# Kernel optimization log

Measured on AMD Instinct MI355X. Metric: run time of the kernel, lower is better.

## Reference

```python
import jax, jax.numpy as jnp
import numpy as np

B, H, E, V, T, EOS = 128, 512, 256, 32000, 32, 0

def setup_inputs() -> dict:
    key = jax.random.key(0)
    ks = jax.random.split(key, 10)
    s_emb = 1.0 / np.sqrt(V)
    s_rnn = 1.0 / np.sqrt(H)
    return {
        "z": jax.random.normal(ks[0], (B, H), jnp.float32),
        "W_emb": jax.random.uniform(ks[1], (E, V), jnp.float32, -s_emb, s_emb),
        "b_emb": jax.random.uniform(ks[2], (E,), jnp.float32, -s_emb, s_emb),
        "W_ih": jax.random.uniform(ks[3], (H, E), jnp.float32, -s_rnn, s_rnn),
        "b_ih": jax.random.uniform(ks[4], (H,), jnp.float32, -s_rnn, s_rnn),
        "W_hh": jax.random.uniform(ks[5], (H, H), jnp.float32, -s_rnn, s_rnn),
        "b_hh": jax.random.uniform(ks[6], (H,), jnp.float32, -s_rnn, s_rnn),
        "W_lin": jax.random.uniform(ks[7], (V, H), jnp.float32, -s_rnn, s_rnn),
        "b_lin": jax.random.uniform(ks[8], (V,), jnp.float32, -s_rnn, s_rnn),
        "train": 0,
    }

def _emit(hidden, W_lin, b_lin):
    # [B,H] @ [H,V] -> log_p [B,V]; greedy (argmax) decode path (train=False)
    log_p = jax.nn.log_softmax(hidden @ W_lin.T + b_lin, axis=-1)
    sample = jnp.argmax(log_p, axis=-1)                       # [B] int
    symb = jax.nn.one_hot(sample, V, dtype=log_p.dtype)       # [B,V]
    lp_tok = jnp.take_along_axis(log_p, sample[:, None], axis=1)[:, 0]
    return symb, lp_tok

def reference(z, W_emb, b_emb, W_ih, b_ih, W_hh, b_hh, W_lin, b_lin, train):
    # step 0: hidden = z, no RNN update
    symb, lp_tok = _emit(z, W_lin, b_lin)
    log_p_sent = lp_tok
    mask = 1.0 - symb[:, EOS]

    def step(carry, _):
        hidden, symb, log_p_sent, mask = carry
        emb = symb @ W_emb.T + b_emb                          # one-hot "embedding" linear
        hidden = jnp.tanh(emb @ W_ih.T + b_ih + hidden @ W_hh.T + b_hh)  # Elman RNN cell
        symb, lp_tok = _emit(hidden, W_lin, b_lin)
        log_p_sent = log_p_sent + mask * lp_tok
        mask = mask * (1.0 - symb[:, EOS])
        return (hidden, symb, log_p_sent, mask), symb

    (_, _, log_p_sent, _), rest = jax.lax.scan(step, (z, symb, log_p_sent, mask), None, length=T - 1)
    sentences = jnp.concatenate([symb[None], rest], axis=0)   # [T,B,V]
    return sentences, log_p_sent
```

## Files before the change

kernel.cpp:

```cpp
#include <hip/hip_runtime.h>
#include <math.h>

constexpr int NB = 128;
constexpr int NH = 512;
constexpr int NE = 256;
constexpr int NV = 32000;
constexpr int NT = 32;
constexpr int NVBW = 1000;

typedef _Float16 half8 __attribute__((ext_vector_type(8)));
typedef float    f32x4 __attribute__((ext_vector_type(4)));

__global__ void f32_to_f16_kernel(const float* __restrict__ src,
                                  _Float16* __restrict__ dst, int n8)
{
    int i = blockIdx.x * 256 + threadIdx.x;
    if (i >= n8) return;
    float4 a = ((const float4*)src)[i * 2];
    float4 b = ((const float4*)src)[i * 2 + 1];
    half8 h = { (_Float16)a.x, (_Float16)a.y, (_Float16)a.z, (_Float16)a.w,
                (_Float16)b.x, (_Float16)b.y, (_Float16)b.z, (_Float16)b.w };
    ((half8*)dst)[i] = h;
}

__global__ __launch_bounds__(512, 1)
void logits_kernel(const _Float16* __restrict__ Ah,
                   const _Float16* __restrict__ Wh,
                   const float* __restrict__ blin,
                   float* __restrict__ pm1, int* __restrict__ pi1,
                   float* __restrict__ pm2, int* __restrict__ pi2,
                   float* __restrict__ ps)
{
    __shared__ _Float16 sm[2][2][128][64];

    const int tid  = threadIdx.x;
    const int w    = tid >> 6;
    const int lane = tid & 63;
    const int wm   = w >> 2;
    const int wn   = w & 3;
    const int vb   = blockIdx.x;
    const int v0   = vb * 128;

    const _Float16* gp[4];
    unsigned ldsoff[4];
#pragma unroll
    for (int c = 0; c < 4; c++) {
        int slot = w * 256 + c * 64 + lane;
        int mat  = slot >> 10;
        int r    = (slot >> 3) & 127;
        int sp   = slot & 7;
        int s    = sp ^ (r & 7);
        const _Float16* base = mat ? (Wh + (size_t)(v0 + r) * NH)
                                   : (Ah + (size_t)r * NH);
        gp[c] = base + s * 8;
        ldsoff[c] = (unsigned)(w * 256 + c * 64) * 16;
    }

#define STAGE(db, k0)                                                          \
    do {                                                                       \
        _Pragma("unroll")                                                      \
        for (int c = 0; c < 4; c++) {                                          \
            __builtin_amdgcn_global_load_lds(                                  \
                (const __attribute__((address_space(1))) unsigned*)(gp[c] + (k0)), \
                (__attribute__((address_space(3))) unsigned*)((char*)&sm[db][0][0][0] + ldsoff[c]), \
                16, 0, 0);                                                     \
        }                                                                      \
    } while (0)

    f32x4 acc[4][2];
#pragma unroll
    for (int mi = 0; mi < 4; mi++)
#pragma unroll
        for (int ni = 0; ni < 2; ni++) acc[mi][ni] = {0.f, 0.f, 0.f, 0.f};

    STAGE(0, 0);
    asm volatile("s_waitcnt vmcnt(0)" ::: "memory");
    __builtin_amdgcn_sched_barrier(0);
    __builtin_amdgcn_s_barrier();

    int db = 0;
    for (int t = 0; t < 8; t++) {
        if (t < 7) STAGE(db ^ 1, (t + 1) * 64);
#pragma unroll
        for (int kk = 0; kk < 2; kk++) {
            const int sbase = kk * 4 + (lane >> 4);
            half8 af[4], bf[2];
#pragma unroll
            for (int mi = 0; mi < 4; mi++) {
                int r = wm * 64 + mi * 16 + (lane & 15);
                af[mi] = *(const half8*)&sm[db][0][r][(sbase ^ (r & 7)) * 8];
            }
#pragma unroll
            for (int ni = 0; ni < 2; ni++) {
                int rb = wn * 32 + ni * 16 + (lane & 15);
                bf[ni] = *(const half8*)&sm[db][1][rb][(sbase ^ (rb & 7)) * 8];
            }
#pragma unroll
            for (int mi = 0; mi < 4; mi++)
#pragma unroll
                for (int ni = 0; ni < 2; ni++)
                    acc[mi][ni] = __builtin_amdgcn_mfma_f32_16x16x32_f16(
                        af[mi], bf[ni], acc[mi][ni], 0, 0, 0);
        }
        asm volatile("s_waitcnt vmcnt(0)" ::: "memory");
        __builtin_amdgcn_sched_barrier(0);
        __builtin_amdgcn_s_barrier();
        db ^= 1;
    }
#undef STAGE

    const int colbase = v0 + wn * 32 + (lane & 15);
    const float bias0 = blin[colbase];
    const float bias1 = blin[colbase + 16];
    const int cidx = vb * 4 + wn;

#pragma unroll
    for (int mi = 0; mi < 4; mi++) {
#pragma unroll
        for (int reg = 0; reg < 4; reg++) {
            const int b = wm * 64 + mi * 16 + (lane >> 4) * 4 + reg;
            const float va = acc[mi][0][reg] + bias0;
            const float vc = acc[mi][1][reg] + bias1;
            float a1, a2; int j1, j2;
            if (va >= vc) { a1 = va; j1 = colbase;      a2 = vc; j2 = colbase + 16; }
            else          { a1 = vc; j1 = colbase + 16; a2 = va; j2 = colbase; }
#pragma unroll
            for (int off = 1; off < 16; off <<= 1) {
                float o1 = __shfl_xor(a1, off), o2 = __shfl_xor(a2, off);
                int   k1 = __shfl_xor(j1, off), k2 = __shfl_xor(j2, off);
                float n1, n2; int m1, m2;
                bool ob = (o1 > a1) || (o1 == a1 && k1 < j1);
                if (ob) {
                    n1 = o1; m1 = k1;
                    bool t2 = (a1 > o2) || (a1 == o2 && j1 < k2);
                    if (t2) { n2 = a1; m2 = j1; } else { n2 = o2; m2 = k2; }
                } else {
                    n1 = a1; m1 = j1;
                    bool t2 = (o1 > a2) || (o1 == a2 && k1 < j2);
                    if (t2) { n2 = o1; m2 = k1; } else { n2 = a2; m2 = j2; }
                }
                a1 = n1; j1 = m1; a2 = n2; j2 = m2;
            }
            float s = __expf(va - a1) + __expf(vc - a1);
#pragma unroll
            for (int off = 1; off < 16; off <<= 1) s += __shfl_xor(s, off);
            if ((lane & 15) == 0) {
                pm1[b * NVBW + cidx] = a1;  pi1[b * NVBW + cidx] = j1;
                pm2[b * NVBW + cidx] = a2;  pi2[b * NVBW + cidx] = j2;
                ps [b * NVBW + cidx] = s;
            }
        }
    }
}

__global__ __launch_bounds__(256, 2)
void emit_rnn_kernel(int t,
                     const float* __restrict__ hid_in,
                     const float* __restrict__ Wlin, const float* __restrict__ blin,
                     const float* __restrict__ pm1, const int* __restrict__ pi1,
                     const float* __restrict__ pm2, const int* __restrict__ pi2,
                     const float* __restrict__ ps,
                     const float* __restrict__ Wemb, const float* __restrict__ bemb,
                     const float* __restrict__ Wih, const float* __restrict__ bih,
                     const float* __restrict__ Whh, const float* __restrict__ bhh,
                     float* __restrict__ hid_out, _Float16* __restrict__ hidh_out,
                     float* __restrict__ lps, float* __restrict__ maskp,
                     float* __restrict__ out)
{
    constexpr float DELTA = 0.01f;
    constexpr int   MAXC  = 32;

    const int b = blockIdx.x, tid = threadIdx.x;
    const int w = tid >> 6, lane = tid & 63;

    __shared__ float red[4];
    __shared__ int   cand[MAXC];
    __shared__ float cval[MAXC];
    __shared__ int   ncand;
    __shared__ int   besti;
    __shared__ float es[NE];
    __shared__ float hs[NH];

    hs[tid]       = hid_in[(size_t)b * NH + tid];
    hs[tid + 256] = hid_in[(size_t)b * NH + tid + 256];
    if (tid == 0) ncand = 0;

    float m = -1e30f;
    for (int c = tid; c < NVBW; c += 256) m = fmaxf(m, pm1[b * NVBW + c]);
#pragma unroll
    for (int off = 1; off < 64; off <<= 1) m = fmaxf(m, __shfl_xor(m, off));
    if (lane == 0) red[w] = m;
    __syncthreads();
    const float gm = fmaxf(fmaxf(red[0], red[1]), fmaxf(red[2], red[3]));
    __syncthreads();

    float s = 0.f;
    for (int c = tid; c < NVBW; c += 256) {
        float p1 = pm1[b * NVBW + c];
        s += ps[b * NVBW + c] * __expf(p1 - gm);
        if (p1 >= gm - DELTA) {
            int pos = atomicAdd(&ncand, 1);
            if (pos < MAXC) cand[pos] = pi1[b * NVBW + c];
        }
        float p2 = pm2[b * NVBW + c];
        if (p2 >= gm - DELTA) {
            int pos = atomicAdd(&ncand, 1);
            if (pos < MAXC) cand[pos] = pi2[b * NVBW + c];
        }
    }
#pragma unroll
    for (int off = 1; off < 64; off <<= 1) s += __shfl_xor(s, off);
    if (lane == 0) red[w] = s;
    __syncthreads();
    const float tot = red[0] + red[1] + red[2] + red[3];
    const int nc = min(ncand, MAXC);

    for (int ci = w; ci < nc; ci += 4) {
        int tok = cand[ci];
        float4 h0 = ((const float4*)hs)[lane * 2];
        float4 h1 = ((const float4*)hs)[lane * 2 + 1];
        const float4* wv = (const float4*)(Wlin + (size_t)tok * NH);
        float4 w0 = wv[lane * 2], w1 = wv[lane * 2 + 1];
        float d = h0.x * w0.x + h0.y * w0.y + h0.z * w0.z + h0.w * w0.w
                + h1.x * w1.x + h1.y * w1.y + h1.z * w1.z + h1.w * w1.w;
#pragma unroll
        for (int off = 1; off < 64; off <<= 1) d += __shfl_xor(d, off);
        if (lane == 0) cval[ci] = d + blin[tok];
    }
    __syncthreads();

    if (tid == 0) {
        float bv = cval[0]; int bi = cand[0];
        for (int ci = 1; ci < nc; ci++)
            if (cval[ci] > bv || (cval[ci] == bv && cand[ci] < bi)) { bv = cval[ci]; bi = cand[ci]; }
        float lp = (bv - gm) - logf(tot);
        float lpv, mk;
        if (t == 0) { lpv = lp; mk = (bi == 0) ? 0.f : 1.f; }
        else {
            lpv = lps[b]; mk = maskp[b];
            lpv += mk * lp;
            mk *= (bi == 0) ? 0.f : 1.f;
        }
        lps[b] = lpv; maskp[b] = mk;
        out[(size_t)t * NB * NV + (size_t)b * NV + bi] = 1.0f;
        if (t == NT - 1) out[(size_t)NT * NB * NV + b] = lpv;
        besti = bi;
    }
    __syncthreads();
    const int gi = besti;

    if (t == NT - 1) return;

    es[tid] = Wemb[(size_t)tid * NV + gi] + bemb[tid];
    __syncthreads();

#pragma unroll
    for (int hh = 0; hh < 2; hh++) {
        int h = tid + hh * 256;
        float acc = bih[h] + bhh[h];
        const float4* wi = (const float4*)(Wih + (size_t)h * NE);
#pragma unroll 4
        for (int e4 = 0; e4 < NE / 4; e4++) {
            float4 ww = wi[e4];
            acc += ww.x * es[e4 * 4] + ww.y * es[e4 * 4 + 1]
                 + ww.z * es[e4 * 4 + 2] + ww.w * es[e4 * 4 + 3];
        }
        const float4* wh = (const float4*)(Whh + (size_t)h * NH);
#pragma unroll 4
        for (int k4 = 0; k4 < NH / 4; k4++) {
            float4 ww = wh[k4];
            acc += ww.x * hs[k4 * 4] + ww.y * hs[k4 * 4 + 1]
                 + ww.z * hs[k4 * 4 + 2] + ww.w * hs[k4 * 4 + 3];
        }
        float v = tanhf(acc);
        hid_out[(size_t)b * NH + h]  = v;
        hidh_out[(size_t)b * NH + h] = (_Float16)v;
    }
}

extern "C" void kernel_launch(void* const* d_in, const int* in_sizes, int n_in,
                              void* d_out, int out_size, void* d_ws, size_t ws_size,
                              hipStream_t stream) {
    const float* z    = (const float*)d_in[0];
    const float* Wemb = (const float*)d_in[1];
    const float* bemb = (const float*)d_in[2];
    const float* Wih  = (const float*)d_in[3];
    const float* bih  = (const float*)d_in[4];
    const float* Whh  = (const float*)d_in[5];
    const float* bhh  = (const float*)d_in[6];
    const float* Wlin = (const float*)d_in[7];
    const float* blin = (const float*)d_in[8];
    float* out = (float*)d_out;

    char* ws = (char*)d_ws;
    _Float16* Wh    = (_Float16*)(ws);
    _Float16* hidh  = (_Float16*)(ws + 32768000);
    _Float16* zh    = (_Float16*)(ws + 32899072);
    float*    hid   = (float*)   (ws + 33030144);
    float*    pm1   = (float*)   (ws + 33292288);
    int*      pi1   = (int*)     (ws + 33804288);
    float*    pm2   = (float*)   (ws + 34316288);
    int*      pi2   = (int*)     (ws + 34828288);
    float*    ps    = (float*)   (ws + 35340288);
    float*    lps   = (float*)   (ws + 35852288);
    float*    maskp = (float*)   (ws + 35852800);

    hipMemsetAsync(d_out, 0, (size_t)NT * NB * NV * sizeof(float), stream);
    f32_to_f16_kernel<<<NV * NH / 8 / 256, 256, 0, stream>>>(Wlin, Wh, NV * NH / 8);
    f32_to_f16_kernel<<<NB * NH / 8 / 256, 256, 0, stream>>>(z, zh, NB * NH / 8);

    for (int t = 0; t < NT; t++) {
        const float*    hin = (t == 0) ? z  : hid;
        const _Float16* ah  = (t == 0) ? zh : hidh;
        logits_kernel<<<250, 512, 0, stream>>>(ah, Wh, blin, pm1, pi1, pm2, pi2, ps);
        emit_rnn_kernel<<<NB, 256, 0, stream>>>(t, hin, Wlin, blin,
                                                pm1, pi1, pm2, pi2, ps,
                                                Wemb, bemb, Wih, bih, Whh, bhh,
                                                hid, hidh, lps, maskp, out);
    }
}
```

Before: 2.992 ms.

## Fuse all decode steps into one persistent cooperative kernel with grid syncs

Replaces the memset, two conversion kernels and 64 per-step launches with a single cooperative kernel of 256 blocks. The blocks zero the output, convert weights to fp16, and then loop over the timesteps, with grid-wide syncs separating the logits GEMM phase from the emit/RNN phase. This removes kernel launch gaps and the per-step launch overhead. In exchange it adds grid-sync latency and narrows the emit phase to 512-thread blocks doing one hidden unit per thread. It also requires that all 256 blocks be co-resident.

```diff
diff --git a/kernel.cpp b/kernel.cpp
--- a/kernel.cpp
+++ b/kernel.cpp
@@ -1,5 +1,8 @@
 #include <hip/hip_runtime.h>
+#include <hip/hip_cooperative_groups.h>
 #include <math.h>
+
+namespace cg = cooperative_groups;
 
 constexpr int NB = 128;
 constexpr int NH = 512;
@@ -11,50 +14,82 @@
 typedef _Float16 half8 __attribute__((ext_vector_type(8)));
 typedef float    f32x4 __attribute__((ext_vector_type(4)));
 
-__global__ void f32_to_f16_kernel(const float* __restrict__ src,
-                                  _Float16* __restrict__ dst, int n8)
+__global__ __launch_bounds__(512, 2)
+void speaker_kernel(const float* __restrict__ z,    const float* __restrict__ Wemb,
+                    const float* __restrict__ bemb, const float* __restrict__ Wih,
+                    const float* __restrict__ bih,  const float* __restrict__ Whh,
+                    const float* __restrict__ bhh,  const float* __restrict__ Wlin,
+                    const float* __restrict__ blin, float* __restrict__ out,
+                    _Float16* __restrict__ Wh, _Float16* __restrict__ hidh,
+                    _Float16* __restrict__ zh, float* __restrict__ hid,
+                    float* __restrict__ pm1, int* __restrict__ pi1,
+                    float* __restrict__ pm2, int* __restrict__ pi2,
+                    float* __restrict__ ps,  float* __restrict__ lps,
+                    float* __restrict__ maskp)
 {
-    int i = blockIdx.x * 256 + threadIdx.x;
-    if (i >= n8) return;
-    float4 a = ((const float4*)src)[i * 2];
-    float4 b = ((const float4*)src)[i * 2 + 1];
-    half8 h = { (_Float16)a.x, (_Float16)a.y, (_Float16)a.z, (_Float16)a.w,
-                (_Float16)b.x, (_Float16)b.y, (_Float16)b.z, (_Float16)b.w };
-    ((half8*)dst)[i] = h;
-}
-
-__global__ __launch_bounds__(512, 1)
-void logits_kernel(const _Float16* __restrict__ Ah,
-                   const _Float16* __restrict__ Wh,
-                   const float* __restrict__ blin,
-                   float* __restrict__ pm1, int* __restrict__ pi1,
-                   float* __restrict__ pm2, int* __restrict__ pi2,
-                   float* __restrict__ ps)
-{
+    cg::grid_group grid = cg::this_grid();
+
     __shared__ _Float16 sm[2][2][128][64];
-
+    __shared__ float red8[8];
+    __shared__ int   cand[32];
+    __shared__ float cval[32];
+    __shared__ int   ncand;
+    __shared__ int   besti;
+    __shared__ float es[NE];
+    __shared__ float hs[NH];
+
+    const int blk  = blockIdx.x;
     const int tid  = threadIdx.x;
+    const int gtid = blk * 512 + tid;
+    constexpr int GT = 256 * 512;
+
+    {
+        const float4 z4 = {0.f, 0.f, 0.f, 0.f};
+        float4* o4 = (float4*)out;
+        for (int i = gtid; i < (NT * NB * NV + NB) / 4; i += GT) o4[i] = z4;
+        for (int i = gtid; i < NV * NH / 8; i += GT) {
+            float4 a = ((const float4*)Wlin)[i * 2];
+            float4 b = ((const float4*)Wlin)[i * 2 + 1];
+            half8 h = { (_Float16)a.x, (_Float16)a.y, (_Float16)a.z, (_Float16)a.w,
+                        (_Float16)b.x, (_Float16)b.y, (_Float16)b.z, (_Float16)b.w };
+            ((half8*)Wh)[i] = h;
+        }
+        for (int i = gtid; i < NB * NH / 8; i += GT) {
+            float4 a = ((const float4*)z)[i * 2];
+            float4 b = ((const float4*)z)[i * 2 + 1];
+            half8 h = { (_Float16)a.x, (_Float16)a.y, (_Float16)a.z, (_Float16)a.w,
+                        (_Float16)b.x, (_Float16)b.y, (_Float16)b.z, (_Float16)b.w };
+            ((half8*)zh)[i] = h;
+        }
+    }
+    __threadfence();
+    grid.sync();
+
     const int w    = tid >> 6;
     const int lane = tid & 63;
-    const int wm   = w >> 2;
-    const int wn   = w & 3;
-    const int vb   = blockIdx.x;
-    const int v0   = vb * 128;
-
-    const _Float16* gp[4];
-    unsigned ldsoff[4];
-#pragma unroll
-    for (int c = 0; c < 4; c++) {
-        int slot = w * 256 + c * 64 + lane;
-        int mat  = slot >> 10;
-        int r    = (slot >> 3) & 127;
-        int sp   = slot & 7;
-        int s    = sp ^ (r & 7);
-        const _Float16* base = mat ? (Wh + (size_t)(v0 + r) * NH)
-                                   : (Ah + (size_t)r * NH);
-        gp[c] = base + s * 8;
-        ldsoff[c] = (unsigned)(w * 256 + c * 64) * 16;
-    }
+
+    for (int t = 0; t < NT; t++) {
+        if (blk < 250) {
+            const _Float16* Ah = (t == 0) ? zh : hidh;
+            const int wm = w >> 2;
+            const int wn = w & 3;
+            const int vb = blk;
+            const int v0 = vb * 128;
+
+            const _Float16* gp[4];
+            unsigned ldsoff[4];
+#pragma unroll
+            for (int c = 0; c < 4; c++) {
+                int slot = w * 256 + c * 64 + lane;
+                int mat  = slot >> 10;
+                int r    = (slot >> 3) & 127;
+                int sp   = slot & 7;
+                int s    = sp ^ (r & 7);
+                const _Float16* base = mat ? (Wh + (size_t)(v0 + r) * NH)
+                                           : (Ah + (size_t)r * NH);
+                gp[c] = base + s * 8;
+                ldsoff[c] = (unsigned)(w * 256 + c * 64) * 16;
+            }
 
 #define STAGE(db, k0)                                                          \
     do {                                                                       \
@@ -67,214 +102,197 @@
         }                                                                      \
     } while (0)
 
-    f32x4 acc[4][2];
-#pragma unroll
-    for (int mi = 0; mi < 4; mi++)
-#pragma unroll
-        for (int ni = 0; ni < 2; ni++) acc[mi][ni] = {0.f, 0.f, 0.f, 0.f};
-
-    STAGE(0, 0);
-    asm volatile("s_waitcnt vmcnt(0)" ::: "memory");
-    __builtin_amdgcn_sched_barrier(0);
-    __builtin_amdgcn_s_barrier();
-
-    int db = 0;
-    for (int t = 0; t < 8; t++) {
-        if (t < 7) STAGE(db ^ 1, (t + 1) * 64);
-#pragma unroll
-        for (int kk = 0; kk < 2; kk++) {
-            const int sbase = kk * 4 + (lane >> 4);
-            half8 af[4], bf[2];
+            f32x4 acc[4][2];
+#pragma unroll
+            for (int mi = 0; mi < 4; mi++)
+#pragma unroll
+                for (int ni = 0; ni < 2; ni++) acc[mi][ni] = {0.f, 0.f, 0.f, 0.f};
+
+            STAGE(0, 0);
+            asm volatile("s_waitcnt vmcnt(0)" ::: "memory");
+            __builtin_amdgcn_sched_barrier(0);
+            __builtin_amdgcn_s_barrier();
+
+            int db = 0;
+            for (int kt = 0; kt < 8; kt++) {
+                if (kt < 7) STAGE(db ^ 1, (kt + 1) * 64);
+#pragma unroll
+                for (int kk = 0; kk < 2; kk++) {
+                    const int sbase = kk * 4 + (lane >> 4);
+                    half8 af[4], bf[2];
+#pragma unroll
+                    for (int mi = 0; mi < 4; mi++) {
+                        int r = wm * 64 + mi * 16 + (lane & 15);
+                        af[mi] = *(const half8*)&sm[db][0][r][(sbase ^ (r & 7)) * 8];
+                    }
+#pragma unroll
+                    for (int ni = 0; ni < 2; ni++) {
+                        int rb = wn * 32 + ni * 16 + (lane & 15);
+                        bf[ni] = *(const half8*)&sm[db][1][rb][(sbase ^ (rb & 7)) * 8];
+                    }
+#pragma unroll
+                    for (int mi = 0; mi < 4; mi++)
+#pragma unroll
+                        for (int ni = 0; ni < 2; ni++)
+                            acc[mi][ni] = __builtin_amdgcn_mfma_f32_16x16x32_f16(
+                                af[mi], bf[ni], acc[mi][ni], 0, 0, 0);
+                }
+                asm volatile("s_waitcnt vmcnt(0)" ::: "memory");
+                __builtin_amdgcn_sched_barrier(0);
+                __builtin_amdgcn_s_barrier();
+                db ^= 1;
+            }
+#undef STAGE
+
+            const int colbase = v0 + wn * 32 + (lane & 15);
+            const float bias0 = blin[colbase];
+            const float bias1 = blin[colbase + 16];
+            const int cidx = vb * 4 + wn;
+
 #pragma unroll
             for (int mi = 0; mi < 4; mi++) {
-                int r = wm * 64 + mi * 16 + (lane & 15);
-                af[mi] = *(const half8*)&sm[db][0][r][(sbase ^ (r & 7)) * 8];
-            }
-#pragma unroll
-            for (int ni = 0; ni < 2; ni++) {
-                int rb = wn * 32 + ni * 16 + (lane & 15);
-                bf[ni] = *(const half8*)&sm[db][1][rb][(sbase ^ (rb & 7)) * 8];
-            }
-#pragma unroll
-            for (int mi = 0; mi < 4; mi++)
-#pragma unroll
-                for (int ni = 0; ni < 2; ni++)
-                    acc[mi][ni] = __builtin_amdgcn_mfma_f32_16x16x32_f16(
-                        af[mi], bf[ni], acc[mi][ni], 0, 0, 0);
+#pragma unroll
+                for (int reg = 0; reg < 4; reg++) {
+                    const int b = wm * 64 + mi * 16 + (lane >> 4) * 4 + reg;
+                    const float va = acc[mi][0][reg] + bias0;
+                    const float vc = acc[mi][1][reg] + bias1;
+                    float a1, a2; int j1, j2;
+                    if (va >= vc) { a1 = va; j1 = colbase;      a2 = vc; j2 = colbase + 16; }
+                    else          { a1 = vc; j1 = colbase + 16; a2 = va; j2 = colbase; }
+#pragma unroll
+                    for (int off = 1; off < 16; off <<= 1) {
+                        float o1 = __shfl_xor(a1, off), o2 = __shfl_xor(a2, off);
+                        int   k1 = __shfl_xor(j1, off), k2 = __shfl_xor(j2, off);
+                        float n1, n2; int m1, m2;
+                        bool ob = (o1 > a1) || (o1 == a1 && k1 < j1);
+                        if (ob) {
+                            n1 = o1; m1 = k1;
+                            bool t2 = (a1 > o2) || (a1 == o2 && j1 < k2);
+                            if (t2) { n2 = a1; m2 = j1; } else { n2 = o2; m2 = k2; }
+                        } else {
+                            n1 = a1; m1 = j1;
+                            bool t2 = (o1 > a2) || (o1 == a2 && k1 < j2);
+                            if (t2) { n2 = o1; m2 = k1; } else { n2 = a2; m2 = j2; }
+                        }
+                        a1 = n1; j1 = m1; a2 = n2; j2 = m2;
+                    }
+                    float s = __expf(va - a1) + __expf(vc - a1);
+#pragma unroll
+                    for (int off = 1; off < 16; off <<= 1) s += __shfl_xor(s, off);
+                    if ((lane & 15) == 0) {
+                        pm1[b * NVBW + cidx] = a1;  pi1[b * NVBW + cidx] = j1;
+                        pm2[b * NVBW + cidx] = a2;  pi2[b * NVBW + cidx] = j2;
+                        ps [b * NVBW + cidx] = s;
+                    }
+                }
+            }
         }
-        asm volatile("s_waitcnt vmcnt(0)" ::: "memory");
-        __builtin_amdgcn_sched_barrier(0);
-        __builtin_amdgcn_s_barrier();
-        db ^= 1;
-    }
-#undef STAGE
-
-    const int colbase = v0 + wn * 32 + (lane & 15);
-    const float bias0 = blin[colbase];
-    const float bias1 = blin[colbase + 16];
-    const int cidx = vb * 4 + wn;
-
-#pragma unroll
-    for (int mi = 0; mi < 4; mi++) {
-#pragma unroll
-        for (int reg = 0; reg < 4; reg++) {
-            const int b = wm * 64 + mi * 16 + (lane >> 4) * 4 + reg;
-            const float va = acc[mi][0][reg] + bias0;
-            const float vc = acc[mi][1][reg] + bias1;
-            float a1, a2; int j1, j2;
-            if (va >= vc) { a1 = va; j1 = colbase;      a2 = vc; j2 = colbase + 16; }
-            else          { a1 = vc; j1 = colbase + 16; a2 = va; j2 = colbase; }
-#pragma unroll
-            for (int off = 1; off < 16; off <<= 1) {
-                float o1 = __shfl_xor(a1, off), o2 = __shfl_xor(a2, off);
-                int   k1 = __shfl_xor(j1, off), k2 = __shfl_xor(j2, off);
-                float n1, n2; int m1, m2;
-                bool ob = (o1 > a1) || (o1 == a1 && k1 < j1);
-                if (ob) {
-                    n1 = o1; m1 = k1;
-                    bool t2 = (a1 > o2) || (a1 == o2 && j1 < k2);
-                    if (t2) { n2 = a1; m2 = j1; } else { n2 = o2; m2 = k2; }
-                } else {
-                    n1 = a1; m1 = j1;
-                    bool t2 = (o1 > a2) || (o1 == a2 && k1 < j2);
-                    if (t2) { n2 = o1; m2 = k1; } else { n2 = a2; m2 = j2; }
-                }
-                a1 = n1; j1 = m1; a2 = n2; j2 = m2;
-            }
-            float s = __expf(va - a1) + __expf(vc - a1);
-#pragma unroll
-            for (int off = 1; off < 16; off <<= 1) s += __shfl_xor(s, off);
-            if ((lane & 15) == 0) {
-                pm1[b * NVBW + cidx] = a1;  pi1[b * NVBW + cidx] = j1;
-                pm2[b * NVBW + cidx] = a2;  pi2[b * NVBW + cidx] = j2;
-                ps [b * NVBW + cidx] = s;
+        __threadfence();
+        grid.sync();
+
+        if (blk < NB) {
+            constexpr float DELTA = 0.01f;
+            constexpr int   MAXC  = 32;
+            const int b = blk;
+            const float* hid_in = (t == 0) ? z : hid;
+
+            hs[tid] = hid_in[(size_t)b * NH + tid];
+            if (tid == 0) ncand = 0;
+            __syncthreads();
+
+            float m_ = -1e30f;
+            for (int c = tid; c < NVBW; c += 512) m_ = fmaxf(m_, pm1[b * NVBW + c]);
+#pragma unroll
+            for (int off = 1; off < 64; off <<= 1) m_ = fmaxf(m_, __shfl_xor(m_, off));
+            if (lane == 0) red8[w] = m_;
+            __syncthreads();
+            const float gmax = fmaxf(fmaxf(fmaxf(red8[0], red8[1]), fmaxf(red8[2], red8[3])),
+                                     fmaxf(fmaxf(red8[4], red8[5]), fmaxf(red8[6], red8[7])));
+            __syncthreads();
+
+            float s = 0.f;
+            for (int c = tid; c < NVBW; c += 512) {
+                float p1 = pm1[b * NVBW + c];
+                s += ps[b * NVBW + c] * __expf(p1 - gmax);
+                if (p1 >= gmax - DELTA) {
+                    int pos = atomicAdd(&ncand, 1);
+                    if (pos < MAXC) cand[pos] = pi1[b * NVBW + c];
+                }
+                float p2 = pm2[b * NVBW + c];
+                if (p2 >= gmax - DELTA) {
+                    int pos = atomicAdd(&ncand, 1);
+                    if (pos < MAXC) cand[pos] = pi2[b * NVBW + c];
+                }
+            }
+#pragma unroll
+            for (int off = 1; off < 64; off <<= 1) s += __shfl_xor(s, off);
+            if (lane == 0) red8[w] = s;
+            __syncthreads();
+            const float tot = ((red8[0] + red8[1]) + (red8[2] + red8[3]))
+                            + ((red8[4] + red8[5]) + (red8[6] + red8[7]));
+            const int nc = min(ncand, MAXC);
+
+            for (int ci = w; ci < nc; ci += 8) {
+                int tok = cand[ci];
+                float4 h0 = ((const float4*)hs)[lane * 2];
+                float4 h1 = ((const float4*)hs)[lane * 2 + 1];
+                const float4* wv = (const float4*)(Wlin + (size_t)tok * NH);
+                float4 w0 = wv[lane * 2], w1 = wv[lane * 2 + 1];
+                float d = h0.x * w0.x + h0.y * w0.y + h0.z * w0.z + h0.w * w0.w
+                        + h1.x * w1.x + h1.y * w1.y + h1.z * w1.z + h1.w * w1.w;
+#pragma unroll
+                for (int off = 1; off < 64; off <<= 1) d += __shfl_xor(d, off);
+                if (lane == 0) cval[ci] = d + blin[tok];
+            }
+            __syncthreads();
+
+            if (tid == 0) {
+                float bv = cval[0]; int bi = cand[0];
+                for (int ci = 1; ci < nc; ci++)
+                    if (cval[ci] > bv || (cval[ci] == bv && cand[ci] < bi)) { bv = cval[ci]; bi = cand[ci]; }
+                float lp = (bv - gmax) - logf(tot);
+                float lpv, mk;
+                if (t == 0) { lpv = lp; mk = (bi == 0) ? 0.f : 1.f; }
+                else {
+                    lpv = lps[b]; mk = maskp[b];
+                    lpv += mk * lp;
+                    mk *= (bi == 0) ? 0.f : 1.f;
+                }
+                lps[b] = lpv; maskp[b] = mk;
+                out[(size_t)t * NB * NV + (size_t)b * NV + bi] = 1.0f;
+                if (t == NT - 1) out[(size_t)NT * NB * NV + b] = lpv;
+                besti = bi;
+            }
+            __syncthreads();
+            const int gi = besti;
+
+            if (t < NT - 1) {
+                if (tid < NE) es[tid] = Wemb[(size_t)tid * NV + gi] + bemb[tid];
+                __syncthreads();
+
+                const int h = tid;
+                float acc = bih[h] + bhh[h];
+                const float4* wi = (const float4*)(Wih + (size_t)h * NE);
+#pragma unroll 4
+                for (int e4 = 0; e4 < NE / 4; e4++) {
+                    float4 ww = wi[e4];
+                    acc += ww.x * es[e4 * 4] + ww.y * es[e4 * 4 + 1]
+                         + ww.z * es[e4 * 4 + 2] + ww.w * es[e4 * 4 + 3];
+                }
+                const float4* wh = (const float4*)(Whh + (size_t)h * NH);
+#pragma unroll 4
+                for (int k4 = 0; k4 < NH / 4; k4++) {
+                    float4 ww = wh[k4];
+                    acc += ww.x * hs[k4 * 4] + ww.y * hs[k4 * 4 + 1]
+                         + ww.z * hs[k4 * 4 + 2] + ww.w * hs[k4 * 4 + 3];
+                }
+                float v = tanhf(acc);
+                hid[(size_t)b * NH + h]  = v;
+                hidh[(size_t)b * NH + h] = (_Float16)v;
             }
         }
-    }
-}
-
-__global__ __launch_bounds__(256, 2)
-void emit_rnn_kernel(int t,
-                     const float* __restrict__ hid_in,
-                     const float* __restrict__ Wlin, const float* __restrict__ blin,
-                     const float* __restrict__ pm1, const int* __restrict__ pi1,
-                     const float* __restrict__ pm2, const int* __restrict__ pi2,
-                     const float* __restrict__ ps,
-                     const float* __restrict__ Wemb, const float* __restrict__ bemb,
-                     const float* __restrict__ Wih, const float* __restrict__ bih,
-                     const float* __restrict__ Whh, const float* __restrict__ bhh,
-                     float* __restrict__ hid_out, _Float16* __restrict__ hidh_out,
-                     float* __restrict__ lps, float* __restrict__ maskp,
-                     float* __restrict__ out)
-{
-    constexpr float DELTA = 0.01f;
-    constexpr int   MAXC  = 32;
-
-    const int b = blockIdx.x, tid = threadIdx.x;
-    const int w = tid >> 6, lane = tid & 63;
-
-    __shared__ float red[4];
-    __shared__ int   cand[MAXC];
-    __shared__ float cval[MAXC];
-    __shared__ int   ncand;
-    __shared__ int   besti;
-    __shared__ float es[NE];
-    __shared__ float hs[NH];
-
-    hs[tid]       = hid_in[(size_t)b * NH + tid];
-    hs[tid + 256] = hid_in[(size_t)b * NH + tid + 256];
-    if (tid == 0) ncand = 0;
-
-    float m = -1e30f;
-    for (int c = tid; c < NVBW; c += 256) m = fmaxf(m, pm1[b * NVBW + c]);
-#pragma unroll
-    for (int off = 1; off < 64; off <<= 1) m = fmaxf(m, __shfl_xor(m, off));
-    if (lane == 0) red[w] = m;
-    __syncthreads();
-    const float gm = fmaxf(fmaxf(red[0], red[1]), fmaxf(red[2], red[3]));
-    __syncthreads();
-
-    float s = 0.f;
-    for (int c = tid; c < NVBW; c += 256) {
-        float p1 = pm1[b * NVBW + c];
-        s += ps[b * NVBW + c] * __expf(p1 - gm);
-        if (p1 >= gm - DELTA) {
-            int pos = atomicAdd(&ncand, 1);
-            if (pos < MAXC) cand[pos] = pi1[b * NVBW + c];
-        }
-        float p2 = pm2[b * NVBW + c];
-        if (p2 >= gm - DELTA) {
-            int pos = atomicAdd(&ncand, 1);
-            if (pos < MAXC) cand[pos] = pi2[b * NVBW + c];
-        }
-    }
-#pragma unroll
-    for (int off = 1; off < 64; off <<= 1) s += __shfl_xor(s, off);
-    if (lane == 0) red[w] = s;
-    __syncthreads();
-    const float tot = red[0] + red[1] + red[2] + red[3];
-    const int nc = min(ncand, MAXC);
-
-    for (int ci = w; ci < nc; ci += 4) {
-        int tok = cand[ci];
-        float4 h0 = ((const float4*)hs)[lane * 2];
-        float4 h1 = ((const float4*)hs)[lane * 2 + 1];
-        const float4* wv = (const float4*)(Wlin + (size_t)tok * NH);
-        float4 w0 = wv[lane * 2], w1 = wv[lane * 2 + 1];
-        float d = h0.x * w0.x + h0.y * w0.y + h0.z * w0.z + h0.w * w0.w
-                + h1.x * w1.x + h1.y * w1.y + h1.z * w1.z + h1.w * w1.w;
-#pragma unroll
-        for (int off = 1; off < 64; off <<= 1) d += __shfl_xor(d, off);
-        if (lane == 0) cval[ci] = d + blin[tok];
-    }
-    __syncthreads();
-
-    if (tid == 0) {
-        float bv = cval[0]; int bi = cand[0];
-        for (int ci = 1; ci < nc; ci++)
-            if (cval[ci] > bv || (cval[ci] == bv && cand[ci] < bi)) { bv = cval[ci]; bi = cand[ci]; }
-        float lp = (bv - gm) - logf(tot);
-        float lpv, mk;
-        if (t == 0) { lpv = lp; mk = (bi == 0) ? 0.f : 1.f; }
-        else {
-            lpv = lps[b]; mk = maskp[b];
-            lpv += mk * lp;
-            mk *= (bi == 0) ? 0.f : 1.f;
-        }
-        lps[b] = lpv; maskp[b] = mk;
-        out[(size_t)t * NB * NV + (size_t)b * NV + bi] = 1.0f;
-        if (t == NT - 1) out[(size_t)NT * NB * NV + b] = lpv;
-        besti = bi;
-    }
-    __syncthreads();
-    const int gi = besti;
-
-    if (t == NT - 1) return;
-
-    es[tid] = Wemb[(size_t)tid * NV + gi] + bemb[tid];
-    __syncthreads();
-
-#pragma unroll
-    for (int hh = 0; hh < 2; hh++) {
-        int h = tid + hh * 256;
-        float acc = bih[h] + bhh[h];
-        const float4* wi = (const float4*)(Wih + (size_t)h * NE);
-#pragma unroll 4
-        for (int e4 = 0; e4 < NE / 4; e4++) {
-            float4 ww = wi[e4];
-            acc += ww.x * es[e4 * 4] + ww.y * es[e4 * 4 + 1]
-                 + ww.z * es[e4 * 4 + 2] + ww.w * es[e4 * 4 + 3];
-        }
-        const float4* wh = (const float4*)(Whh + (size_t)h * NH);
-#pragma unroll 4
-        for (int k4 = 0; k4 < NH / 4; k4++) {
-            float4 ww = wh[k4];
-            acc += ww.x * hs[k4 * 4] + ww.y * hs[k4 * 4 + 1]
-                 + ww.z * hs[k4 * 4 + 2] + ww.w * hs[k4 * 4 + 3];
-        }
-        float v = tanhf(acc);
-        hid_out[(size_t)b * NH + h]  = v;
-        hidh_out[(size_t)b * NH + h] = (_Float16)v;
+        __threadfence();
+        grid.sync();
     }
 }
 
@@ -305,17 +323,13 @@
     float*    lps   = (float*)   (ws + 35852288);
     float*    maskp = (float*)   (ws + 35852800);
 
-    hipMemsetAsync(d_out, 0, (size_t)NT * NB * NV * sizeof(float), stream);
-    f32_to_f16_kernel<<<NV * NH / 8 / 256, 256, 0, stream>>>(Wlin, Wh, NV * NH / 8);
-    f32_to_f16_kernel<<<NB * NH / 8 / 256, 256, 0, stream>>>(z, zh, NB * NH / 8);
-
-    for (int t = 0; t < NT; t++) {
-        const float*    hin = (t == 0) ? z  : hid;
-        const _Float16* ah  = (t == 0) ? zh : hidh;
-        logits_kernel<<<250, 512, 0, stream>>>(ah, Wh, blin, pm1, pi1, pm2, pi2, ps);
-        emit_rnn_kernel<<<NB, 256, 0, stream>>>(t, hin, Wlin, blin,
-                                                pm1, pi1, pm2, pi2, ps,
-                                                Wemb, bemb, Wih, bih, Whh, bhh,
-                                                hid, hidh, lps, maskp, out);
-    }
+    void* args[] = {
+        (void*)&z, (void*)&Wemb, (void*)&bemb, (void*)&Wih, (void*)&bih,
+        (void*)&Whh, (void*)&bhh, (void*)&Wlin, (void*)&blin, (void*)&out,
+        (void*)&Wh, (void*)&hidh, (void*)&zh, (void*)&hid,
+        (void*)&pm1, (void*)&pi1, (void*)&pm2, (void*)&pi2, (void*)&ps,
+        (void*)&lps, (void*)&maskp
+    };
+    hipLaunchCooperativeKernel((void*)speaker_kernel, dim3(256), dim3(512),
+                               args, 0, stream);
 }
```

New measurement: 7.947 ms. 2.66x slower.
